# Optimization experiments

Hardware: AMD Instinct MI355X
Metric: run time of the kernel (lower is better)

Reference implementation:

```python
import jax, jax.numpy as jnp
import numpy as np

D, H = 1024, 2048
N_STEPS = 2
T0, T1 = 0.0, 1.0


def setup_inputs() -> dict:
    key = jax.random.key(0)
    ks = jax.random.split(key, 5)
    s_in = 1.0 / np.sqrt(D)
    s_h = 1.0 / np.sqrt(H)
    return {
        "x0": jax.random.normal(ks[0], (D,), jnp.float32),
        "W1": jax.random.normal(ks[1], (D, H), jnp.float32) * s_in,
        "b1": jnp.zeros((H,), jnp.float32),
        "wt": jax.random.normal(ks[2], (H,), jnp.float32) * 0.1,
        "W2": jax.random.normal(ks[3], (H, H), jnp.float32) * s_h,
        "b2": jnp.zeros((H,), jnp.float32),
        "W3": jax.random.normal(ks[4], (H, D), jnp.float32) * s_h,
        "b3": jnp.zeros((D,), jnp.float32),
    }


def reference(x0, W1, b1, wt, W2, b2, W3, b3):
    dtype = x0.dtype

    def velocity(t, x):
        # 3-layer tanh MLP velocity field with additive time embedding
        h1 = jnp.tanh(x @ W1 + b1 + t * wt)
        h2 = jnp.tanh(h1 @ W2 + b2)
        return h2 @ W3 + b3

    def vel_and_div(t, x):
        # Mirror of _compute_velocity_and_divergence: linearize + vmap(jvp)
        # over identity to get the full Jacobian, then take its trace.
        v, jvp_fun = jax.linearize(lambda z: velocity(t, z), x)
        cols = jax.vmap(jvp_fun)(jnp.eye(D, dtype=dtype))  # [D, D]
        return v, jnp.trace(cols)

    def aug_dyn(t, x):
        v, div = vel_and_div(t, x)
        return v, -div  # (dx/dt, dlogq/dt)

    # Standard-normal base distribution log_prob at x0
    log2pi = jnp.log(jnp.asarray(2.0 * np.pi, dtype=dtype))
    logq0 = -0.5 * jnp.sum(x0 * x0) - 0.5 * D * log2pi

    dt = jnp.asarray((T1 - T0) / N_STEPS, dtype=dtype)

    def rk4_step(carry, i):
        x, logq = carry
        t = T0 + i * dt
        v1, dl1 = aug_dyn(t, x)
        v2, dl2 = aug_dyn(t + 0.5 * dt, x + 0.5 * dt * v1)
        v3, dl3 = aug_dyn(t + 0.5 * dt, x + 0.5 * dt * v2)
        v4, dl4 = aug_dyn(t + dt, x + dt * v3)
        x_new = x + (dt / 6.0) * (v1 + 2.0 * v2 + 2.0 * v3 + v4)
        logq_new = logq + (dt / 6.0) * (dl1 + 2.0 * dl2 + 2.0 * dl3 + dl4)
        return (x_new, logq_new), None

    (x1, logq1), _ = jax.lax.scan(
        rk4_step, (x0, logq0), jnp.arange(N_STEPS, dtype=dtype)
    )
    # concat [x1 (D,), logq1 ()] -> (D+1,) for a single output array
    return jnp.concatenate([x1, logq1[None]])
```

## Files before the change

kernel.cpp:

```cpp
#include <hip/hip_runtime.h>
#include <math.h>

#define DD 1024
#define HH 2048
#define NCB 256

typedef float f32x4 __attribute__((ext_vector_type(4)));
typedef short short8 __attribute__((ext_vector_type(8)));

__device__ __forceinline__ float b2f(unsigned short u) {
    return __uint_as_float(((unsigned int)u) << 16);
}
__device__ __forceinline__ unsigned short f2b(float f) {
    unsigned int x = __float_as_uint(f);
    unsigned int r = (x + 0x7FFFu + ((x >> 16) & 1u)) >> 16;
    return (unsigned short)r;
}
__device__ __forceinline__ float ald(const float* p) {
    return __hip_atomic_load(p, __ATOMIC_RELAXED, __HIP_MEMORY_SCOPE_AGENT);
}
__device__ __forceinline__ void ast(float* p, float v) {
    __hip_atomic_store(p, v, __ATOMIC_RELAXED, __HIP_MEMORY_SCOPE_AGENT);
}

__global__ __launch_bounds__(256) void k_tr(const float* __restrict__ W1,
                                            const float* __restrict__ W2,
                                            const float* __restrict__ W3,
                                            unsigned short* __restrict__ W1T,
                                            unsigned short* __restrict__ W2T,
                                            unsigned short* __restrict__ W3T,
                                            unsigned short* __restrict__ W3b,
                                            unsigned* __restrict__ sync) {
    __shared__ float tile[64][65];
    const int b = blockIdx.x, t = threadIdx.x;
    if (b == 0) {
        #pragma unroll
        for (int q = 0; q < 18; ++q) {
            int i = t + q * 256;
            if (i < 4368) sync[i] = 0u;
        }
    }
    const float* in; unsigned short* out; int R, C, bx, by;
    bool isW3 = false;
    if (b < 512)       { int bb = b;        in = W1; out = W1T; R = DD; C = HH; bx = bb & 31; by = bb >> 5; }
    else if (b < 1536) { int bb = b - 512;  in = W2; out = W2T; R = HH; C = HH; bx = bb & 31; by = bb >> 5; }
    else               { int bb = b - 1536; in = W3; out = W3T; R = HH; C = DD; bx = bb & 15; by = bb >> 4; isW3 = true; }
    const int c0 = bx * 64, r0 = by * 64;
    const int cc = t & 63, rb = t >> 6;
    #pragma unroll
    for (int p = 0; p < 16; ++p) {
        int rr = p * 4 + rb;
        float v = in[(size_t)(r0 + rr) * C + c0 + cc];
        tile[rr][cc] = v;
        if (isW3) W3b[(size_t)(r0 + rr) * DD + c0 + cc] = f2b(v);
    }
    __syncthreads();
    #pragma unroll
    for (int p = 0; p < 16; ++p) {
        int rr = p * 4 + rb;
        out[(size_t)(c0 + rr) * R + r0 + cc] = f2b(tile[cc][rr]);
    }
}

__global__ __launch_bounds__(256) void k_gemmP(const unsigned short* __restrict__ W1T,
                                               const unsigned short* __restrict__ W3b,
                                               const float* __restrict__ W2,
                                               const float* __restrict__ b3,
                                               const float* __restrict__ x0,
                                               unsigned short* __restrict__ Mb,
                                               unsigned short* __restrict__ Pb,
                                               float* __restrict__ c1,
                                               float* __restrict__ A1g) {
    __shared__ unsigned short At[64][72];
    __shared__ unsigned short Bt[128][72];
    const int b = blockIdx.x, t = threadIdx.x;
    const int m0 = (b & 31) * 64;
    const int k0 = (b >> 5) * 128;
    const int wv = t >> 6, l = t & 63;
    const int fr = l & 15, fg = l >> 4;
    const int ra = t & 63, ha = t >> 6;
    const int rb2 = t & 127, hb = t >> 7;
    const bool do_aux = ((b >> 5) == 0) && (t < 64);
    float c1acc = 0.f, a1acc = 0.f;

    f32x4 acc[4][2] = {};
    for (int i0 = 0; i0 < DD; i0 += 64) {
        {
            const float4* sa = (const float4*)(W1T + (size_t)(m0 + ra) * DD + i0 + ha * 16);
            float4 a0 = sa[0], a1 = sa[1];
            const float4* sb = (const float4*)(W3b + (size_t)(k0 + rb2) * DD + i0 + hb * 32);
            float4 b0 = sb[0], b1 = sb[1], b2v = sb[2], b3v = sb[3];
            float4* da = (float4*)&At[ra][ha * 16];
            da[0] = a0; da[1] = a1;
            float4* db = (float4*)&Bt[rb2][hb * 32];
            db[0] = b0; db[1] = b1; db[2] = b2v; db[3] = b3v;
        }
        __syncthreads();
        if (do_aux) {
            #pragma unroll
            for (int i = 0; i < 64; ++i) {
                float w1v = b2f(At[t][i]);
                c1acc += w1v * b3[i0 + i];
                a1acc += w1v * x0[i0 + i];
            }
        }
        #pragma unroll
        for (int kk = 0; kk < 2; ++kk) {
            short8 af[4], bf[2];
            #pragma unroll
            for (int a = 0; a < 4; ++a)
                af[a] = *(const short8*)&At[a * 16 + fr][kk * 32 + fg * 8];
            #pragma unroll
            for (int bq = 0; bq < 2; ++bq)
                bf[bq] = *(const short8*)&Bt[wv * 32 + bq * 16 + fr][kk * 32 + fg * 8];
            #pragma unroll
            for (int a = 0; a < 4; ++a)
                #pragma unroll
                for (int bq = 0; bq < 2; ++bq)
                    acc[a][bq] = __builtin_amdgcn_mfma_f32_16x16x32_bf16(af[a], bf[bq], acc[a][bq], 0, 0, 0);
        }
        __syncthreads();
    }
    if (do_aux) { c1[m0 + t] = c1acc; A1g[m0 + t] = a1acc; }
    #pragma unroll
    for (int a = 0; a < 4; ++a) {
        #pragma unroll
        for (int bq = 0; bq < 2; ++bq) {
            #pragma unroll
            for (int j = 0; j < 4; ++j) {
                int row = m0 + a * 16 + fg * 4 + j;
                int col = k0 + wv * 32 + bq * 16 + fr;
                size_t idx = (size_t)row * HH + col;
                float m = acc[a][bq][j];
                Mb[idx] = f2b(m);
                Pb[idx] = f2b(m * W2[idx]);
            }
        }
    }
}

__device__ __forceinline__ void garrive(unsigned* sync, int b, unsigned g) {
    __syncthreads();
    if (threadIdx.x == 0) {
        asm volatile("s_waitcnt vmcnt(0)" ::: "memory");
        __hip_atomic_store(&sync[b << 4], g, __ATOMIC_RELAXED, __HIP_MEMORY_SCOPE_AGENT);
    }
}
__device__ __forceinline__ void gwait(unsigned* sync, unsigned g) {
    if (threadIdx.x < 64) {
        while (true) {
            bool ok = true;
            #pragma unroll
            for (int k = 0; k < 4; ++k) {
                unsigned f = __hip_atomic_load(&sync[(threadIdx.x + (k << 6)) << 4],
                                               __ATOMIC_RELAXED, __HIP_MEMORY_SCOPE_AGENT);
                ok &= (f >= g);
            }
            if (!__any((int)(!ok))) break;
            __builtin_amdgcn_s_sleep(1);
        }
    }
    __syncthreads();
}
__device__ __forceinline__ void gbar(unsigned* sync, int b, unsigned g) {
    garrive(sync, b, g);
    gwait(sync, g);
}

__global__ __launch_bounds__(256, 1) void k_chain(
    const unsigned short* __restrict__ Mb,
    const unsigned short* __restrict__ Pb,
    const unsigned short* __restrict__ W2T,
    const unsigned short* __restrict__ W3T,
    const float* __restrict__ x0,
    const float* __restrict__ b1, const float* __restrict__ wt,
    const float* __restrict__ b2, const float* __restrict__ b3,
    const float* __restrict__ c1, const float* __restrict__ A1g,
    float* __restrict__ h1_g, float* __restrict__ h2_g, float* __restrict__ hacc_g,
    float* __restrict__ out,
    unsigned* __restrict__ sync) {
    __shared__ unsigned short Ms[8][2048];
    __shared__ unsigned short Ps[8][2048];
    __shared__ unsigned short Qs[8][2048];
    __shared__ float vecH[2048];
    __shared__ float vecW[2048];
    __shared__ float wred[4];
    const int t = threadIdx.x, b = blockIdx.x;
    const int wib = t >> 6, lane = t & 63;
    const int gw2 = (b << 3) + (wib << 1);
    const int jx = (b << 2) + wib;
    unsigned g = 0;

    const unsigned short* mp = Mb + (size_t)gw2 * HH;
    const unsigned short* pp = Pb + (size_t)gw2 * HH;
    const unsigned short* qp = W2T + (size_t)gw2 * HH;

    const float bb1_0 = b1[gw2], bb1_1 = b1[gw2 + 1];
    const float wt_0 = wt[gw2], wt_1 = wt[gw2 + 1];
    const float bb2_0 = b2[gw2], bb2_1 = b2[gw2 + 1];
    const float c1_0 = c1[gw2], c1_1 = c1[gw2 + 1];

    float A1_0 = 0.f, A1_1 = 0.f;
    float u0 = 0.f, u1 = 0.f;
    float hc0 = 0.f, hc1 = 0.f;
    float wdiv = 0.f;

    float logq_r = 0.f;
    if (b == 0 && wib == 0) {
        float ssum = 0.f;
        #pragma unroll
        for (int q = 0; q < 16; ++q) { float xv = x0[lane + (q << 6)]; ssum += xv * xv; }
        #pragma unroll
        for (int o = 1; o < 64; o <<= 1) ssum += __shfl_xor(ssum, o, 64);
        logq_r = -0.5f * ssum - 0.5f * 1024.0f * 1.8378770664093453f;
    }

    {
        A1_0 = A1g[gw2]; A1_1 = A1g[gw2 + 1];
        float h0 = tanhf(A1_0 + bb1_0);
        float h1v = tanhf(A1_1 + bb1_1);
        u0 = 1.f - h0 * h0; u1 = 1.f - h1v * h1v;
        if (lane == 0) { ast(h1_g + gw2, h0); ast(h1_g + gw2 + 1, h1v); }
    }
    garrive(sync, b, ++g);
    #pragma unroll
    for (int rep = 0; rep < 4; ++rep) {
        const int idx = rep * 512 + lane * 8;
        *(short8*)&Qs[wib * 2][idx]     = *(const short8*)(qp + idx);
        *(short8*)&Qs[wib * 2 + 1][idx] = *(const short8*)(qp + HH + idx);
    }
    gwait(sync, g);

    #pragma unroll
    for (int q = 0; q < 8; ++q) {
        int i = t + (q << 8);
        vecH[i] = ald(h1_g + i);
    }
    __syncthreads();
    {
        float a0 = 0.f, a1 = 0.f;
        #pragma unroll
        for (int rep = 0; rep < 4; ++rep) {
            const int idx = rep * 512 + lane * 8;
            float4 hA = *(const float4*)(vecH + idx);
            float4 hB = *(const float4*)(vecH + idx + 4);
            float hv[8] = {hA.x, hA.y, hA.z, hA.w, hB.x, hB.y, hB.z, hB.w};
            short8 r0 = *(const short8*)&Qs[wib * 2][idx];
            short8 r1 = *(const short8*)&Qs[wib * 2 + 1][idx];
            #pragma unroll
            for (int e = 0; e < 8; ++e) {
                a0 += b2f((unsigned short)r0[e]) * hv[e];
                a1 += b2f((unsigned short)r1[e]) * hv[e];
            }
        }
        #pragma unroll
        for (int o = 1; o < 64; o <<= 1) {
            a0 += __shfl_xor(a0, o, 64); a1 += __shfl_xor(a1, o, 64);
        }
        float q0 = tanhf(a0 + bb2_0), q1 = tanhf(a1 + bb2_1);
        hc0 += (1.f / 12.f) * q0; hc1 += (1.f / 12.f) * q1;
        if (lane == 0) {
            ast(h2_g + gw2, q0); ast(h2_g + gw2 + 1, q1);
        }
    }
    garrive(sync, b, ++g);
    #pragma unroll
    for (int rep = 0; rep < 4; ++rep) {
        const int idx = rep * 512 + lane * 8;
        *(short8*)&Ms[wib * 2][idx]     = *(const short8*)(mp + idx);
        *(short8*)&Ms[wib * 2 + 1][idx] = *(const short8*)(mp + HH + idx);
        *(short8*)&Ps[wib * 2][idx]     = *(const short8*)(pp + idx);
        *(short8*)&Ps[wib * 2 + 1][idx] = *(const short8*)(pp + HH + idx);
    }
    gwait(sync, g);

    for (int s = 1; s < 8; ++s) {
        const int ss = s & 3;
        const float tcur = (s >> 2) * 0.5f + ((ss == 0) ? 0.f : (ss == 3) ? 0.5f : 0.25f);

        {
            #pragma unroll
            for (int q = 0; q < 8; ++q) {
                int i = t + (q << 8);
                float h2v = ald(h2_g + i);
                float sv = (ss == 0) ? ald(hacc_g + i) : h2v;
                vecH[i] = sv;
                vecW[i] = 1.f - h2v * h2v;
            }
            __syncthreads();
            float md0 = 0.f, md1 = 0.f, pd0 = 0.f, pd1 = 0.f;
            #pragma unroll
            for (int rep = 0; rep < 4; ++rep) {
                const int idx = rep * 512 + lane * 8;
                float4 hA = *(const float4*)(vecH + idx);
                float4 hB = *(const float4*)(vecH + idx + 4);
                float4 wA = *(const float4*)(vecW + idx);
                float4 wB = *(const float4*)(vecW + idx + 4);
                float hv[8] = {hA.x, hA.y, hA.z, hA.w, hB.x, hB.y, hB.z, hB.w};
                float wv[8] = {wA.x, wA.y, wA.z, wA.w, wB.x, wB.y, wB.z, wB.w};
                short8 m0v = *(const short8*)&Ms[wib * 2][idx];
                short8 m1v = *(const short8*)&Ms[wib * 2 + 1][idx];
                short8 p0v = *(const short8*)&Ps[wib * 2][idx];
                short8 p1v = *(const short8*)&Ps[wib * 2 + 1][idx];
                #pragma unroll
                for (int e = 0; e < 8; ++e) {
                    md0 += b2f((unsigned short)m0v[e]) * hv[e];
                    md1 += b2f((unsigned short)m1v[e]) * hv[e];
                    pd0 += b2f((unsigned short)p0v[e]) * wv[e];
                    pd1 += b2f((unsigned short)p1v[e]) * wv[e];
                }
            }
            #pragma unroll
            for (int o = 1; o < 64; o <<= 1) {
                md0 += __shfl_xor(md0, o, 64); md1 += __shfl_xor(md1, o, 64);
                pd0 += __shfl_xor(pd0, o, 64); pd1 += __shfl_xor(pd1, o, 64);
            }
            const int sp = (s - 1) & 3;
            const float cprev = (sp == 1 || sp == 2) ? (1.f / 6.f) : (1.f / 12.f);
            wdiv += cprev * (u0 * pd0 + u1 * pd1);
            float pre0, pre1;
            if (ss == 0) {
                A1_0 += md0 + 0.5f * c1_0; A1_1 += md1 + 0.5f * c1_1;
                pre0 = A1_0 + bb1_0 + tcur * wt_0; pre1 = A1_1 + bb1_1 + tcur * wt_1;
            } else {
                const float a = (ss == 3) ? 0.5f : 0.25f;
                pre0 = A1_0 + a * (md0 + c1_0) + bb1_0 + tcur * wt_0;
                pre1 = A1_1 + a * (md1 + c1_1) + bb1_1 + tcur * wt_1;
            }
            float h0 = tanhf(pre0), h1v = tanhf(pre1);
            u0 = 1.f - h0 * h0; u1 = 1.f - h1v * h1v;
            if (lane == 0) { ast(h1_g + gw2, h0); ast(h1_g + gw2 + 1, h1v); }
        }
        gbar(sync, b, ++g);

        #pragma unroll
        for (int q = 0; q < 8; ++q) {
            int i = t + (q << 8);
            vecH[i] = ald(h1_g + i);
        }
        __syncthreads();
        {
            float a0 = 0.f, a1 = 0.f;
            #pragma unroll
            for (int rep = 0; rep < 4; ++rep) {
                const int idx = rep * 512 + lane * 8;
                float4 hA = *(const float4*)(vecH + idx);
                float4 hB = *(const float4*)(vecH + idx + 4);
                float hv[8] = {hA.x, hA.y, hA.z, hA.w, hB.x, hB.y, hB.z, hB.w};
                short8 r0 = *(const short8*)&Qs[wib * 2][idx];
                short8 r1 = *(const short8*)&Qs[wib * 2 + 1][idx];
                #pragma unroll
                for (int e = 0; e < 8; ++e) {
                    a0 += b2f((unsigned short)r0[e]) * hv[e];
                    a1 += b2f((unsigned short)r1[e]) * hv[e];
                }
            }
            #pragma unroll
            for (int o = 1; o < 64; o <<= 1) {
                a0 += __shfl_xor(a0, o, 64); a1 += __shfl_xor(a1, o, 64);
            }
            float q0 = tanhf(a0 + bb2_0), q1 = tanhf(a1 + bb2_1);
            const float cs = (ss == 1 || ss == 2) ? (1.f / 6.f) : (1.f / 12.f);
            hc0 += cs * q0; hc1 += cs * q1;
            if (lane == 0) {
                ast(h2_g + gw2, q0); ast(h2_g + gw2 + 1, q1);
                if (ss == 3) { ast(hacc_g + gw2, hc0); ast(hacc_g + gw2 + 1, hc1); }
            }
        }
        gbar(sync, b, ++g);
    }

    {
        #pragma unroll
        for (int q = 0; q < 8; ++q) {
            int i = t + (q << 8);
            float h2v = ald(h2_g + i);
            vecH[i] = ald(hacc_g + i);
            vecW[i] = 1.f - h2v * h2v;
        }
        __syncthreads();
        float pd0 = 0.f, pd1 = 0.f, xo = 0.f;
        const unsigned short* Vr = W3T + (size_t)jx * HH;
        #pragma unroll
        for (int rep = 0; rep < 4; ++rep) {
            const int idx = rep * 512 + lane * 8;
            float4 cA = *(const float4*)(vecH + idx);
            float4 cB = *(const float4*)(vecH + idx + 4);
            float4 wA = *(const float4*)(vecW + idx);
            float4 wB = *(const float4*)(vecW + idx + 4);
            float cv[8] = {cA.x, cA.y, cA.z, cA.w, cB.x, cB.y, cB.z, cB.w};
            float wv[8] = {wA.x, wA.y, wA.z, wA.w, wB.x, wB.y, wB.z, wB.w};
            short8 p0v = *(const short8*)&Ps[wib * 2][idx];
            short8 p1v = *(const short8*)&Ps[wib * 2 + 1][idx];
            short8 vv = *(const short8*)(Vr + idx);
            #pragma unroll
            for (int e = 0; e < 8; ++e) {
                pd0 += b2f((unsigned short)p0v[e]) * wv[e];
                pd1 += b2f((unsigned short)p1v[e]) * wv[e];
                xo  += b2f((unsigned short)vv[e]) * cv[e];
            }
        }
        #pragma unroll
        for (int o = 1; o < 64; o <<= 1) {
            pd0 += __shfl_xor(pd0, o, 64); pd1 += __shfl_xor(pd1, o, 64);
            xo += __shfl_xor(xo, o, 64);
        }
        wdiv += (1.f / 12.f) * (u0 * pd0 + u1 * pd1);
        if (lane == 0) {
            out[jx] = x0[jx] + xo + b3[jx];
            wred[wib] = wdiv;
        }
    }
    __syncthreads();
    if (t == 0) {
        float dsum = wred[0] + wred[1] + wred[2] + wred[3];
        atomicAdd((float*)(sync + 4096 + (b & 15) * 16), dsum);
        asm volatile("s_waitcnt vmcnt(0)" ::: "memory");
        atomicAdd(sync + 4352, 1u);
    }
    if (b == 0 && wib == 0) {
        if (lane == 0) {
            while (__hip_atomic_load(sync + 4352, __ATOMIC_RELAXED, __HIP_MEMORY_SCOPE_AGENT) < NCB)
                __builtin_amdgcn_s_sleep(2);
        }
        float v = 0.f;
        if (lane < 16) {
            unsigned du = __hip_atomic_load(sync + 4096 + lane * 16,
                                            __ATOMIC_RELAXED, __HIP_MEMORY_SCOPE_AGENT);
            v = __uint_as_float(du);
        }
        #pragma unroll
        for (int o = 1; o < 64; o <<= 1) v += __shfl_xor(v, o, 64);
        if (lane == 0) out[DD] = logq_r - v;
    }
}

extern "C" void kernel_launch(void* const* d_in, const int* in_sizes, int n_in,
                              void* d_out, int out_size, void* d_ws, size_t ws_size,
                              hipStream_t stream) {
    const float* x0 = (const float*)d_in[0];
    const float* W1 = (const float*)d_in[1];
    const float* b1 = (const float*)d_in[2];
    const float* wt = (const float*)d_in[3];
    const float* W2 = (const float*)d_in[4];
    const float* b2 = (const float*)d_in[5];
    const float* W3 = (const float*)d_in[6];
    const float* b3 = (const float*)d_in[7];
    float* out = (float*)d_out;

    char* ws = (char*)d_ws;
    const size_t MB = 1024 * 1024;
    unsigned short* Pb  = (unsigned short*)(ws);
    unsigned short* W2T = (unsigned short*)(ws + 8 * MB);
    unsigned short* W3T = (unsigned short*)(ws + 16 * MB);
    unsigned short* Mb  = (unsigned short*)(ws + 20 * MB);
    unsigned short* W1T = (unsigned short*)(ws + 28 * MB);
    unsigned short* W3b = (unsigned short*)(ws + 32 * MB);
    float* fb = (float*)(ws + 36 * MB);
    float* c1      = fb;
    float* A1g     = fb + 2048;
    float* h1_g    = fb + 4096;
    float* h2_g    = fb + 6144;
    float* hacc_g  = fb + 8192;
    unsigned* sync = (unsigned*)(fb + 10240);

    k_tr<<<2048, 256, 0, stream>>>(W1, W2, W3, W1T, W2T, W3T, W3b, sync);
    k_gemmP<<<512, 256, 0, stream>>>(W1T, W3b, W2, b3, x0, Mb, Pb, c1, A1g);
    k_chain<<<NCB, 256, 0, stream>>>(Mb, Pb, W2T, W3T, x0, b1, wt, b2, b3, c1, A1g,
                                     h1_g, h2_g, hacc_g, out, sync);
}
```

Baseline: 153.8 us.

## Compute P = M*W2 inside chain kernel and batch transpose jobs per block

Stops materializing the bf16 P matrix in the GEMM epilogue. Instead, the chain kernel reads fp32 W2 rows directly and multiplies them by M while staging into shared memory. This removes an 8 MB write plus its later read, at the cost of a 16 MB fp32 W2 read inside the persistent kernel, in a phase that overlaps the grid barrier wait. The transpose kernel also drops from 2048 to 512 blocks, each looping over four tiles, which cuts block launch overhead but reduces parallelism.

```diff
diff --git a/kernel.cpp b/kernel.cpp
--- a/kernel.cpp
+++ b/kernel.cpp
@@ -40,35 +40,37 @@
             if (i < 4368) sync[i] = 0u;
         }
     }
-    const float* in; unsigned short* out; int R, C, bx, by;
-    bool isW3 = false;
-    if (b < 512)       { int bb = b;        in = W1; out = W1T; R = DD; C = HH; bx = bb & 31; by = bb >> 5; }
-    else if (b < 1536) { int bb = b - 512;  in = W2; out = W2T; R = HH; C = HH; bx = bb & 31; by = bb >> 5; }
-    else               { int bb = b - 1536; in = W3; out = W3T; R = HH; C = DD; bx = bb & 15; by = bb >> 4; isW3 = true; }
-    const int c0 = bx * 64, r0 = by * 64;
     const int cc = t & 63, rb = t >> 6;
-    #pragma unroll
-    for (int p = 0; p < 16; ++p) {
-        int rr = p * 4 + rb;
-        float v = in[(size_t)(r0 + rr) * C + c0 + cc];
-        tile[rr][cc] = v;
-        if (isW3) W3b[(size_t)(r0 + rr) * DD + c0 + cc] = f2b(v);
-    }
-    __syncthreads();
-    #pragma unroll
-    for (int p = 0; p < 16; ++p) {
-        int rr = p * 4 + rb;
-        out[(size_t)(c0 + rr) * R + r0 + cc] = f2b(tile[cc][rr]);
+    for (int q = 0; q < 4; ++q) {
+        int job = b + 512 * q;
+        const float* in; unsigned short* out; int R, C, bx, by;
+        bool isW3 = false;
+        if (job < 512)       { int bb = job;        in = W1; out = W1T; R = DD; C = HH; bx = bb & 31; by = bb >> 5; }
+        else if (job < 1536) { int bb = job - 512;  in = W2; out = W2T; R = HH; C = HH; bx = bb & 31; by = bb >> 5; }
+        else                 { int bb = job - 1536; in = W3; out = W3T; R = HH; C = DD; bx = bb & 15; by = bb >> 4; isW3 = true; }
+        const int c0 = bx * 64, r0 = by * 64;
+        #pragma unroll
+        for (int p = 0; p < 16; ++p) {
+            int rr = p * 4 + rb;
+            float v = in[(size_t)(r0 + rr) * C + c0 + cc];
+            tile[rr][cc] = v;
+            if (isW3) W3b[(size_t)(r0 + rr) * DD + c0 + cc] = f2b(v);
+        }
+        __syncthreads();
+        #pragma unroll
+        for (int p = 0; p < 16; ++p) {
+            int rr = p * 4 + rb;
+            out[(size_t)(c0 + rr) * R + r0 + cc] = f2b(tile[cc][rr]);
+        }
+        __syncthreads();
     }
 }
 
 __global__ __launch_bounds__(256) void k_gemmP(const unsigned short* __restrict__ W1T,
                                                const unsigned short* __restrict__ W3b,
-                                               const float* __restrict__ W2,
                                                const float* __restrict__ b3,
                                                const float* __restrict__ x0,
                                                unsigned short* __restrict__ Mb,
-                                               unsigned short* __restrict__ Pb,
                                                float* __restrict__ c1,
                                                float* __restrict__ A1g) {
     __shared__ unsigned short At[64][72];
@@ -130,10 +132,7 @@
             for (int j = 0; j < 4; ++j) {
                 int row = m0 + a * 16 + fg * 4 + j;
                 int col = k0 + wv * 32 + bq * 16 + fr;
-                size_t idx = (size_t)row * HH + col;
-                float m = acc[a][bq][j];
-                Mb[idx] = f2b(m);
-                Pb[idx] = f2b(m * W2[idx]);
+                Mb[(size_t)row * HH + col] = f2b(acc[a][bq][j]);
             }
         }
     }
@@ -169,7 +168,7 @@
 
 __global__ __launch_bounds__(256, 1) void k_chain(
     const unsigned short* __restrict__ Mb,
-    const unsigned short* __restrict__ Pb,
+    const float* __restrict__ W2,
     const unsigned short* __restrict__ W2T,
     const unsigned short* __restrict__ W3T,
     const float* __restrict__ x0,
@@ -192,7 +191,7 @@
     unsigned g = 0;
 
     const unsigned short* mp = Mb + (size_t)gw2 * HH;
-    const unsigned short* pp = Pb + (size_t)gw2 * HH;
+    const float* w2p = W2 + (size_t)gw2 * HH;
     const unsigned short* qp = W2T + (size_t)gw2 * HH;
 
     const float bb1_0 = b1[gw2], bb1_1 = b1[gw2 + 1];
@@ -267,10 +266,24 @@
     #pragma unroll
     for (int rep = 0; rep < 4; ++rep) {
         const int idx = rep * 512 + lane * 8;
-        *(short8*)&Ms[wib * 2][idx]     = *(const short8*)(mp + idx);
-        *(short8*)&Ms[wib * 2 + 1][idx] = *(const short8*)(mp + HH + idx);
-        *(short8*)&Ps[wib * 2][idx]     = *(const short8*)(pp + idx);
-        *(short8*)&Ps[wib * 2 + 1][idx] = *(const short8*)(pp + HH + idx);
+        short8 m0v = *(const short8*)(mp + idx);
+        short8 m1v = *(const short8*)(mp + HH + idx);
+        float4 wa0 = *(const float4*)(w2p + idx);
+        float4 wa1 = *(const float4*)(w2p + idx + 4);
+        float4 wb0 = *(const float4*)(w2p + HH + idx);
+        float4 wb1 = *(const float4*)(w2p + HH + idx + 4);
+        float w0v[8] = {wa0.x, wa0.y, wa0.z, wa0.w, wa1.x, wa1.y, wa1.z, wa1.w};
+        float w1v[8] = {wb0.x, wb0.y, wb0.z, wb0.w, wb1.x, wb1.y, wb1.z, wb1.w};
+        short8 p0v, p1v;
+        #pragma unroll
+        for (int e = 0; e < 8; ++e) {
+            p0v[e] = (short)f2b(b2f((unsigned short)m0v[e]) * w0v[e]);
+            p1v[e] = (short)f2b(b2f((unsigned short)m1v[e]) * w1v[e]);
+        }
+        *(short8*)&Ms[wib * 2][idx]     = m0v;
+        *(short8*)&Ms[wib * 2 + 1][idx] = m1v;
+        *(short8*)&Ps[wib * 2][idx]     = p0v;
+        *(short8*)&Ps[wib * 2 + 1][idx] = p1v;
     }
     gwait(sync, g);
 
@@ -450,13 +463,12 @@
 
     char* ws = (char*)d_ws;
     const size_t MB = 1024 * 1024;
-    unsigned short* Pb  = (unsigned short*)(ws);
-    unsigned short* W2T = (unsigned short*)(ws + 8 * MB);
-    unsigned short* W3T = (unsigned short*)(ws + 16 * MB);
-    unsigned short* Mb  = (unsigned short*)(ws + 20 * MB);
-    unsigned short* W1T = (unsigned short*)(ws + 28 * MB);
-    unsigned short* W3b = (unsigned short*)(ws + 32 * MB);
-    float* fb = (float*)(ws + 36 * MB);
+    unsigned short* W2T = (unsigned short*)(ws);
+    unsigned short* W3T = (unsigned short*)(ws + 8 * MB);
+    unsigned short* Mb  = (unsigned short*)(ws + 12 * MB);
+    unsigned short* W1T = (unsigned short*)(ws + 20 * MB);
+    unsigned short* W3b = (unsigned short*)(ws + 24 * MB);
+    float* fb = (float*)(ws + 28 * MB);
     float* c1      = fb;
     float* A1g     = fb + 2048;
     float* h1_g    = fb + 4096;
@@ -464,8 +476,8 @@
     float* hacc_g  = fb + 8192;
     unsigned* sync = (unsigned*)(fb + 10240);
 
-    k_tr<<<2048, 256, 0, stream>>>(W1, W2, W3, W1T, W2T, W3T, W3b, sync);
-    k_gemmP<<<512, 256, 0, stream>>>(W1T, W3b, W2, b3, x0, Mb, Pb, c1, A1g);
-    k_chain<<<NCB, 256, 0, stream>>>(Mb, Pb, W2T, W3T, x0, b1, wt, b2, b3, c1, A1g,
+    k_tr<<<512, 256, 0, stream>>>(W1, W2, W3, W1T, W2T, W3T, W3b, sync);
+    k_gemmP<<<512, 256, 0, stream>>>(W1T, W3b, b3, x0, Mb, c1, A1g);
+    k_chain<<<NCB, 256, 0, stream>>>(Mb, W2, W2T, W3T, x0, b1, wt, b2, b3, c1, A1g,
                                      h1_g, h2_g, hacc_g, out, sync);
 }
```

After: 167.7 us. 1.09x slower.
